# Optimization experiments

Hardware: AMD Instinct MI355X
Metric: run time of the kernel (lower is better)

## Reference

```python
import jax, jax.numpy as jnp
import numpy as np

SIGMA = 0.5
TAU = 2.0


def setup_inputs() -> dict:
    key = jax.random.key(0)
    k1, k2, k3 = jax.random.split(key, 3)
    B = 32
    Dx, Dy, Dz, C = 128, 128, 128, 16
    # ray origins in voxel coordinates [0, D-1]
    ray_origin = jax.random.uniform(k1, (B, 3), dtype=jnp.float32) * 127.0
    # unit ray directions (scan() normalizes directions)
    d = jax.random.normal(k2, (B, 3), dtype=jnp.float32)
    ray_dir = d / jnp.linalg.norm(d, axis=-1, keepdims=True)
    memory = jax.random.normal(k3, (Dx, Dy, Dz, C), dtype=jnp.float32)
    return {"ray_origin": ray_origin, "ray_dir": ray_dir, "memory": memory}


def _read(ray_origin, ray_dir, memory):
    Dx, Dy, Dz, C = memory.shape
    # flat grid coordinates [N, 3], N = Dx*Dy*Dz
    gx, gy, gz = jnp.meshgrid(jnp.arange(Dx, dtype=jnp.float32),
                              jnp.arange(Dy, dtype=jnp.float32),
                              jnp.arange(Dz, dtype=jnp.float32), indexing="ij")
    x = jnp.stack([gx, gy, gz], axis=-1).reshape(-1, 3)  # [N, 3]
    mem = memory.reshape(-1, C)                           # [N, C]

    # t = dx . d  computed without materializing dx = x - o per ray:
    # t[n,b] = x[n].d[b] - o[b].d[b]
    t = x @ ray_dir.T - jnp.sum(ray_origin * ray_dir, axis=-1)[None, :]   # [N, B]
    dx2 = (jnp.sum(x * x, axis=-1)[:, None]
           - 2.0 * (x @ ray_origin.T)
           + jnp.sum(ray_origin * ray_origin, axis=-1)[None, :])          # [N, B]
    # r2 = |dx - t d|^2 = |dx|^2 - 2 t^2 + t^2 |d|^2 (exact for any d)
    d2 = jnp.sum(ray_dir * ray_dir, axis=-1)[None, :]                     # [1, B]
    r2 = dx2 - 2.0 * t * t + t * t * d2                                   # [N, B]

    kern = jnp.exp(-r2 / (2.0 * SIGMA ** 2)) * jnp.exp(-jnp.maximum(t, 0.0) / TAU)
    # weighted reduce over the grid: out[b,c] = sum_n kern[n,b] * mem[n,c]
    return jnp.einsum("nb,nc->bc", kern, mem)


def reference(ray_origin, ray_dir, memory):
    return _read(ray_origin, ray_dir, memory)
```

## Files before the change

### kernel.cpp

```cpp
#include <hip/hip_runtime.h>
#include <math.h>


constexpr int BRAYS  = 32;
constexpr int DGRID  = 128;
constexpr int NCHUNK = 32;
constexpr int PLANES = DGRID / NCHUNK;
constexpr int NTHR   = 256;
constexpr int NBLK   = BRAYS * NCHUNK;

__global__ __launch_bounds__(NTHR)
void hpm_tube(const float* __restrict__ ray_o,
              const float* __restrict__ ray_d,
              const float* __restrict__ mem,
              float* __restrict__ part)
{
    const int tid   = threadIdx.x;
    const int b     = blockIdx.x & (BRAYS - 1);
    const int chunk = blockIdx.x >> 5;
    const int k0    = chunk * PLANES;

    const float ox = ray_o[b*3+0], oy = ray_o[b*3+1], oz = ray_o[b*3+2];
    const float dx = ray_d[b*3+0], dy = ray_d[b*3+1], dz = ray_d[b*3+2];
    const float ax = fabsf(dx), ay = fabsf(dy), az = fabsf(dz);

    int a;
    if (ax >= ay && ax >= az) a = 0; else if (ay >= az) a = 1; else a = 2;
    const int p1 = (a == 0) ? 1 : 0;
    const int p2 = (a == 2) ? 1 : 2;

    const float o3[3] = {ox, oy, oz};
    const float d3[3] = {dx, dy, dz};
    const int   st[3] = {DGRID * DGRID * 16, DGRID * 16, 16};

    const float oa = o3[a],  da = d3[a];
    const float o1 = o3[p1], d1 = d3[p1];
    const float o2 = o3[p2], d2 = d3[p2];
    const int   sa = st[a],  s1 = st[p1], s2 = st[p2];
    const float inv_da = 1.0f / da;
    const float q = 2.0f - (dx*dx + dy*dy + dz*dz);

    const int u = tid >> 4;
    const int v = tid & 15;

    float acc[16];
    #pragma unroll
    for (int c = 0; c < 16; ++c) acc[c] = 0.0f;

    #pragma unroll
    for (int i = 0; i < PLANES; ++i) {
        const int   k  = k0 + i;
        const float tk = ((float)k - oa) * inv_da;
        if (tk > 46.0f) continue;

        const float yc = o1 + tk * d1;
        const float zc = o2 + tk * d2;
        const int y = (int)floorf(yc) - 7 + u;
        const int z = (int)floorf(zc) - 7 + v;

        const float e0 = (float)k - oa;
        const float e1 = (float)y - o1;
        const float e2 = (float)z - o2;
        const float t   = fmaf(e0, da, fmaf(e1, d1, e2 * d2));
        const float ee  = fmaf(e0, e0, fmaf(e1, e1, e2 * e2));
        const float r2  = fmaf(-q * t, t, ee);
        const float arg = fmaf(fmaxf(t, 0.0f), -0.5f, -2.0f * r2);

        if (arg > -20.0f && ((unsigned)y < 128u) && ((unsigned)z < 128u)) {
            const float w = __expf(arg);
            const float4* row = reinterpret_cast<const float4*>(
                mem + (size_t)k * sa + (size_t)y * s1 + (size_t)z * s2);
            const float4 m0 = row[0], m1 = row[1], m2 = row[2], m3 = row[3];
            acc[ 0] = fmaf(w, m0.x, acc[ 0]); acc[ 1] = fmaf(w, m0.y, acc[ 1]);
            acc[ 2] = fmaf(w, m0.z, acc[ 2]); acc[ 3] = fmaf(w, m0.w, acc[ 3]);
            acc[ 4] = fmaf(w, m1.x, acc[ 4]); acc[ 5] = fmaf(w, m1.y, acc[ 5]);
            acc[ 6] = fmaf(w, m1.z, acc[ 6]); acc[ 7] = fmaf(w, m1.w, acc[ 7]);
            acc[ 8] = fmaf(w, m2.x, acc[ 8]); acc[ 9] = fmaf(w, m2.y, acc[ 9]);
            acc[10] = fmaf(w, m2.z, acc[10]); acc[11] = fmaf(w, m2.w, acc[11]);
            acc[12] = fmaf(w, m3.x, acc[12]); acc[13] = fmaf(w, m3.y, acc[13]);
            acc[14] = fmaf(w, m3.z, acc[14]); acc[15] = fmaf(w, m3.w, acc[15]);
        }
    }

    const int lane = tid & 63;
    float r[16];
    #pragma unroll
    for (int c = 0; c < 16; ++c) r[c] = acc[c];

#define FOLD(MASK, HALF)                                        \
    {                                                           \
        const bool hi = (lane & (MASK)) != 0;                   \
        _Pragma("unroll")                                       \
        for (int i = 0; i < (HALF); ++i) {                      \
            const float give = hi ? r[i] : r[i + (HALF)];       \
            const float keep = hi ? r[i + (HALF)] : r[i];       \
            r[i] = keep + __shfl_xor(give, (MASK), 64);         \
        }                                                       \
    }
    FOLD(1, 8)
    FOLD(2, 4)
    FOLD(4, 2)
    FOLD(8, 1)
#undef FOLD
    float sum = r[0];
    sum += __shfl_xor(sum, 16, 64);
    sum += __shfl_xor(sum, 32, 64);
    const int l4 = lane & 15;
    const int ch = ((l4 & 1) << 3) | ((l4 & 2) << 1) | ((l4 & 4) >> 1) | ((l4 & 8) >> 3);

    __shared__ float ws[4][16];
    if (lane < 16) ws[tid >> 6][ch] = sum;
    __syncthreads();

    if (tid < 16) {
        const float p = ws[0][tid] + ws[1][tid] + ws[2][tid] + ws[3][tid];
        part[(chunk * BRAYS + b) * 16 + tid] = p;
    }
}

__global__ __launch_bounds__(512)
void hpm_reduce(const float* __restrict__ part, float* __restrict__ out)
{
    const int e = threadIdx.x;
    float s = 0.0f;
    #pragma unroll
    for (int k = 0; k < NCHUNK; ++k)
        s += part[k * (BRAYS * 16) + e];
    out[e] = s;
}

extern "C" void kernel_launch(void* const* d_in, const int* in_sizes, int n_in,
                              void* d_out, int out_size, void* d_ws, size_t ws_size,
                              hipStream_t stream)
{
    const float* ray_o = (const float*)d_in[0];
    const float* ray_d = (const float*)d_in[1];
    const float* mem   = (const float*)d_in[2];
    float* out  = (float*)d_out;
    float* part = (float*)d_ws;

    hipLaunchKernelGGL(hpm_tube, dim3(NBLK), dim3(NTHR), 0, stream,
                       ray_o, ray_d, mem, part);
    hipLaunchKernelGGL(hpm_reduce, dim3(1), dim3(512), 0, stream,
                       part, out);
}
```

Baseline: 12.08 us.

## Fuse final reduction into main kernel via per-block completion flags

Adds an extra block to the tube kernel that spins on per-block flags until all partial sums are written, then reduces them into the output and resets the flags. This removes the second kernel launch and its launch gap. It relies on the extra block being co-resident with or scheduled after the producer blocks; with 1025 blocks this is likely fine, but it uses relaxed atomics without explicit release/acquire fences, which is a memory-ordering risk. It falls back to two launches if the workspace is too small.

```diff
diff --git a/kernel.cpp b/kernel.cpp
--- a/kernel.cpp
+++ b/kernel.cpp
@@ -8,14 +8,39 @@
 constexpr int PLANES = DGRID / NCHUNK;
 constexpr int NTHR   = 256;
 constexpr int NBLK   = BRAYS * NCHUNK;
+constexpr unsigned MAGIC = 0x5EEDBEEFu;
+
+#define AT_LOAD(p)     __hip_atomic_load((p), __ATOMIC_RELAXED, __HIP_MEMORY_SCOPE_AGENT)
+#define AT_STORE(p, v) __hip_atomic_store((p), (v), __ATOMIC_RELAXED, __HIP_MEMORY_SCOPE_AGENT)
 
 __global__ __launch_bounds__(NTHR)
 void hpm_tube(const float* __restrict__ ray_o,
               const float* __restrict__ ray_d,
               const float* __restrict__ mem,
-              float* __restrict__ part)
+              float* __restrict__ part,
+              unsigned* __restrict__ flags,
+              float* __restrict__ out,
+              int fanin)
 {
-    const int tid   = threadIdx.x;
+    const int tid = threadIdx.x;
+
+    if (blockIdx.x == NBLK) {
+        for (int j = tid; j < NBLK; j += NTHR)
+            while (AT_LOAD(&flags[j]) != MAGIC) {  }
+        __syncthreads();
+
+        for (int e = tid; e < BRAYS * 16; e += NTHR) {
+            float s = 0.0f;
+            #pragma unroll
+            for (int k = 0; k < NCHUNK; ++k)
+                s += AT_LOAD(&part[k * (BRAYS * 16) + e]);
+            out[e] = s;
+        }
+        for (int j = tid; j < NBLK; j += NTHR)
+            AT_STORE(&flags[j], 0u);
+        return;
+    }
+
     const int b     = blockIdx.x & (BRAYS - 1);
     const int chunk = blockIdx.x >> 5;
     const int k0    = chunk * PLANES;
@@ -114,7 +139,12 @@
 
     if (tid < 16) {
         const float p = ws[0][tid] + ws[1][tid] + ws[2][tid] + ws[3][tid];
-        part[(chunk * BRAYS + b) * 16 + tid] = p;
+        AT_STORE(&part[(chunk * BRAYS + b) * 16 + tid], p);
+    }
+
+    if (fanin) {
+        __syncthreads();
+        if (tid == 0) AT_STORE(&flags[chunk * BRAYS + b], MAGIC);
     }
 }
 
@@ -137,10 +167,20 @@
     const float* ray_d = (const float*)d_in[1];
     const float* mem   = (const float*)d_in[2];
     float* out  = (float*)d_out;
-    float* part = (float*)d_ws;
 
-    hipLaunchKernelGGL(hpm_tube, dim3(NBLK), dim3(NTHR), 0, stream,
-                       ray_o, ray_d, mem, part);
-    hipLaunchKernelGGL(hpm_reduce, dim3(1), dim3(512), 0, stream,
-                       part, out);
+    float*    part  = (float*)d_ws;
+    unsigned* flags = (unsigned*)((char*)d_ws + NBLK * 64);
+
+    const size_t need = (size_t)NBLK * 64 + NBLK * sizeof(unsigned);
+    const int fanin = (ws_size >= need) ? 1 : 0;
+
+    if (fanin) {
+        hipLaunchKernelGGL(hpm_tube, dim3(NBLK + 1), dim3(NTHR), 0, stream,
+                           ray_o, ray_d, mem, part, flags, out, 1);
+    } else {
+        hipLaunchKernelGGL(hpm_tube, dim3(NBLK), dim3(NTHR), 0, stream,
+                           ray_o, ray_d, mem, part, flags, out, 0);
+        hipLaunchKernelGGL(hpm_reduce, dim3(1), dim3(512), 0, stream,
+                           part, out);
+    }
 }
```

New measurement: 11.82 us. 1.02x faster.
